# Performance work log

Measured on AMD Instinct MI355X. Metric: run time of the kernel, lower is better.

## Reference

```python
import jax, jax.numpy as jnp
import numpy as np

VOCAB, D = 100000, 300
B, L = 256, 1000
H, C = 512, 5


def setup_inputs() -> dict:
    key = jax.random.key(0)
    ks = jax.random.split(key, 9)
    emb = jax.random.normal(ks[0], (VOCAB, D), dtype=jnp.float32) * 0.1
    W1 = jax.random.normal(ks[1], (D, H), dtype=jnp.float32) * (1.0 / np.sqrt(D))
    b1 = jnp.zeros((H,), dtype=jnp.float32)
    W2 = jax.random.normal(ks[2], (H, H), dtype=jnp.float32) * (1.0 / np.sqrt(H))
    b2 = jnp.zeros((H,), dtype=jnp.float32)
    W3 = jax.random.normal(ks[3], (H, C), dtype=jnp.float32) * (1.0 / np.sqrt(H))
    b3 = jnp.zeros((C,), dtype=jnp.float32)
    docs = jax.random.randint(ks[4], (B, L), 0, VOCAB, dtype=jnp.int32)
    doc_lens = jax.random.randint(ks[5], (B,), 1, L + 1, dtype=jnp.int32)
    return {"embeddings": emb, "W1": W1, "b1": b1, "W2": W2, "b2": b2,
            "W3": W3, "b3": b3, "docs": docs, "doc_lens": doc_lens}


def reference(embeddings, W1, b1, W2, b2, W3, b3, docs, doc_lens):
    # Fused gather + segment-mean: [B, L, D] -> [B, D]
    gathered = embeddings[docs]                       # [B, L, D]
    avg = gathered.sum(axis=1) / doc_lens.astype(jnp.float32)[:, None]  # [B, D]
    # MLP: in -> hidden (ReLU) -> hidden (ReLU) -> classes
    h = jax.nn.relu(avg @ W1 + b1)
    h = jax.nn.relu(h @ W2 + b2)
    return h @ W3 + b3                                # [B, C]
```

## Files before the change

### kernel.cpp

```cpp
#include <hip/hip_runtime.h>

#define VOCAB 100000
#define D     300
#define B     256
#define L     1000
#define H     512
#define C     5

#define D4    (D / 4)
#define NG    8
#define GL    80
#define RPG   (L / NG)
#define NT    (NG * GL)
#define KS1   (D / 4)
#define KS2   (H / 4)

__global__ __launch_bounds__(NT, 3) void dan_fused_kernel(
    const float* __restrict__ emb, const int* __restrict__ docs,
    const int* __restrict__ dlen,
    const float* __restrict__ W1, const float* __restrict__ b1,
    const float* __restrict__ W2, const float* __restrict__ b2,
    const float* __restrict__ W3, const float* __restrict__ b3,
    float* __restrict__ out) {
  const int b = blockIdx.x;
  const int t = threadIdx.x;

  __shared__ int    sidx[L];
  __shared__ float4 sred[NG][D4];
  __shared__ float4 s_in4[D4];
  __shared__ float  s_h1[H];
  __shared__ float  s_h2[H];
  __shared__ float  s_comb[4][H];
  __shared__ float  s_len;

  if (t < L / 4)
    reinterpret_cast<int4*>(sidx)[t] =
        reinterpret_cast<const int4*>(docs + (size_t)b * L)[t];
  if (t == NT - 1) s_len = (float)dlen[b];
  __syncthreads();

  const int g = t / GL;
  const int lane = t - g * GL;
  if (lane < D4) {
    float ax = 0.f, ay = 0.f, az = 0.f, aw = 0.f;
    const int base = g * RPG;
#pragma unroll 2
    for (int i = 0; i < RPG; i += 5) {
      const float4 v0 =
          reinterpret_cast<const float4*>(emb + (size_t)sidx[base + i + 0] * D)[lane];
      const float4 v1 =
          reinterpret_cast<const float4*>(emb + (size_t)sidx[base + i + 1] * D)[lane];
      const float4 v2 =
          reinterpret_cast<const float4*>(emb + (size_t)sidx[base + i + 2] * D)[lane];
      const float4 v3 =
          reinterpret_cast<const float4*>(emb + (size_t)sidx[base + i + 3] * D)[lane];
      const float4 v4 =
          reinterpret_cast<const float4*>(emb + (size_t)sidx[base + i + 4] * D)[lane];
      ax += v0.x; ay += v0.y; az += v0.z; aw += v0.w;
      ax += v1.x; ay += v1.y; az += v1.z; aw += v1.w;
      ax += v2.x; ay += v2.y; az += v2.z; aw += v2.w;
      ax += v3.x; ay += v3.y; az += v3.z; aw += v3.w;
      ax += v4.x; ay += v4.y; az += v4.z; aw += v4.w;
    }
    sred[g][lane] = make_float4(ax, ay, az, aw);
  }
  __syncthreads();

  if (t < D4) {
    float ax = 0.f, ay = 0.f, az = 0.f, aw = 0.f;
#pragma unroll
    for (int gg = 0; gg < NG; ++gg) {
      const float4 v = sred[gg][t];
      ax += v.x; ay += v.y; az += v.z; aw += v.w;
    }
    const float inv = 1.f / s_len;
    s_in4[t] = make_float4(ax * inv, ay * inv, az * inv, aw * inv);
  }
  __syncthreads();

  const float* s_in = reinterpret_cast<const float*>(s_in4);
  const int cg = t & 127;
  const int ks = (t >> 7) & 3;

  if (t < 512) {
    float ax = 0.f, ay = 0.f, az = 0.f, aw = 0.f;
    const int k0 = ks * KS1;
#pragma unroll 1
    for (int i = 0; i < KS1; i += 15) {
      float4 w[15];
#pragma unroll
      for (int j = 0; j < 15; ++j)
        w[j] = *reinterpret_cast<const float4*>(&W1[(k0 + i + j) * H + 4 * cg]);
#pragma unroll
      for (int j = 0; j < 15; ++j) {
        const float x = s_in[k0 + i + j];
        ax += x * w[j].x; ay += x * w[j].y; az += x * w[j].z; aw += x * w[j].w;
      }
    }
    *reinterpret_cast<float4*>(&s_comb[ks][4 * cg]) =
        make_float4(ax, ay, az, aw);
  }
  __syncthreads();
  if (t < H) {
    const float v =
        s_comb[0][t] + s_comb[1][t] + s_comb[2][t] + s_comb[3][t] + b1[t];
    s_h1[t] = fmaxf(v, 0.f);
  }
  __syncthreads();

  if (t < 512) {
    float ax = 0.f, ay = 0.f, az = 0.f, aw = 0.f;
    const int k0 = ks * KS2;
#pragma unroll 1
    for (int i = 0; i < KS2; i += 16) {
      float4 w[16];
#pragma unroll
      for (int j = 0; j < 16; ++j)
        w[j] = *reinterpret_cast<const float4*>(&W2[(k0 + i + j) * H + 4 * cg]);
#pragma unroll
      for (int j = 0; j < 16; ++j) {
        const float x = s_h1[k0 + i + j];
        ax += x * w[j].x; ay += x * w[j].y; az += x * w[j].z; aw += x * w[j].w;
      }
    }
    *reinterpret_cast<float4*>(&s_comb[ks][4 * cg]) =
        make_float4(ax, ay, az, aw);
  }
  __syncthreads();
  if (t < H) {
    const float v =
        s_comb[0][t] + s_comb[1][t] + s_comb[2][t] + s_comb[3][t] + b2[t];
    s_h2[t] = fmaxf(v, 0.f);
  }
  __syncthreads();

  const int wv = t >> 6;
  const int ln = t & 63;
  if (wv < C) {
    float a = 0.f;
#pragma unroll
    for (int i = 0; i < H / 64; ++i) {
      const int h = i * 64 + ln;
      a += s_h2[h] * W3[h * C + wv];
    }
#pragma unroll
    for (int off = 32; off > 0; off >>= 1) a += __shfl_down(a, off);
    if (ln == 0) out[b * C + wv] = a + b3[wv];
  }
}

extern "C" void kernel_launch(void* const* d_in, const int* in_sizes, int n_in,
                              void* d_out, int out_size, void* d_ws,
                              size_t ws_size, hipStream_t stream) {
  const float* emb  = (const float*)d_in[0];
  const float* W1   = (const float*)d_in[1];
  const float* b1   = (const float*)d_in[2];
  const float* W2   = (const float*)d_in[3];
  const float* b2   = (const float*)d_in[4];
  const float* W3   = (const float*)d_in[5];
  const float* b3   = (const float*)d_in[6];
  const int*   docs = (const int*)d_in[7];
  const int*   dlen = (const int*)d_in[8];
  float* out = (float*)d_out;

  dan_fused_kernel<<<B, NT, 0, stream>>>(emb, docs, dlen, W1, b1, W2, b2, W3,
                                         b3, out);
}
```

Baseline: 68.65 us.

## Split fused kernel into gather-mean and batched tiled MLP kernels

Splits the single per-document fused kernel into four kernels: gather+mean, a layer-1 GEMM, a layer-2 GEMM and a small head. The GEMM kernels tile 16 documents by 32 output columns, so each W1/W2 load is reused across 16 documents instead of every block streaming the full weight matrices. The gather loop is also made explicitly double-buffered with sched barriers to keep more loads in flight. The cost is three extra kernel launches and round-trips of the intermediates through global workspace memory.

```diff
diff --git a/kernel.cpp b/kernel.cpp
--- a/kernel.cpp
+++ b/kernel.cpp
@@ -7,61 +7,67 @@
 #define H     512
 #define C     5
 
-#define D4    (D / 4)
+#define D4    75
 #define NG    8
 #define GL    80
-#define RPG   (L / NG)
-#define NT    (NG * GL)
-#define KS1   (D / 4)
-#define KS2   (H / 4)
-
-__global__ __launch_bounds__(NT, 3) void dan_fused_kernel(
-    const float* __restrict__ emb, const int* __restrict__ docs,
-    const int* __restrict__ dlen,
-    const float* __restrict__ W1, const float* __restrict__ b1,
-    const float* __restrict__ W2, const float* __restrict__ b2,
-    const float* __restrict__ W3, const float* __restrict__ b3,
-    float* __restrict__ out) {
+#define RPG   125
+#define NT    640
+
+#define WS_AVG 0
+#define WS_H1  (B * D)
+#define WS_H2  (WS_H1 + B * H)
+
+__global__ __launch_bounds__(NT)
+__attribute__((amdgpu_waves_per_eu(2, 3)))
+void gather_mean_kernel(const float* __restrict__ emb,
+                        const int* __restrict__ docs,
+                        const int* __restrict__ dlen,
+                        float* __restrict__ avg) {
   const int b = blockIdx.x;
   const int t = threadIdx.x;
 
   __shared__ int    sidx[L];
   __shared__ float4 sred[NG][D4];
-  __shared__ float4 s_in4[D4];
-  __shared__ float  s_h1[H];
-  __shared__ float  s_h2[H];
-  __shared__ float  s_comb[4][H];
-  __shared__ float  s_len;
 
   if (t < L / 4)
     reinterpret_cast<int4*>(sidx)[t] =
         reinterpret_cast<const int4*>(docs + (size_t)b * L)[t];
-  if (t == NT - 1) s_len = (float)dlen[b];
   __syncthreads();
 
   const int g = t / GL;
   const int lane = t - g * GL;
+  const float4* ep4 = reinterpret_cast<const float4*>(emb);
+
   if (lane < D4) {
+    const int base = g * RPG;
     float ax = 0.f, ay = 0.f, az = 0.f, aw = 0.f;
-    const int base = g * RPG;
-#pragma unroll 2
-    for (int i = 0; i < RPG; i += 5) {
-      const float4 v0 =
-          reinterpret_cast<const float4*>(emb + (size_t)sidx[base + i + 0] * D)[lane];
-      const float4 v1 =
-          reinterpret_cast<const float4*>(emb + (size_t)sidx[base + i + 1] * D)[lane];
-      const float4 v2 =
-          reinterpret_cast<const float4*>(emb + (size_t)sidx[base + i + 2] * D)[lane];
-      const float4 v3 =
-          reinterpret_cast<const float4*>(emb + (size_t)sidx[base + i + 3] * D)[lane];
-      const float4 v4 =
-          reinterpret_cast<const float4*>(emb + (size_t)sidx[base + i + 4] * D)[lane];
-      ax += v0.x; ay += v0.y; az += v0.z; aw += v0.w;
-      ax += v1.x; ay += v1.y; az += v1.z; aw += v1.w;
-      ax += v2.x; ay += v2.y; az += v2.z; aw += v2.w;
-      ax += v3.x; ay += v3.y; az += v3.z; aw += v3.w;
-      ax += v4.x; ay += v4.y; az += v4.z; aw += v4.w;
-    }
+    float4 va[5], vb[5];
+
+    auto loadb = [&](float4* v, int off) {
+#pragma unroll
+      for (int j = 0; j < 5; ++j) {
+        const int r = sidx[base + off + j] * D4 + lane;
+        v[j] = ep4[r];
+      }
+    };
+    auto accb = [&](const float4* v) {
+#pragma unroll
+      for (int j = 0; j < 5; ++j) {
+        ax += v[j].x; ay += v[j].y; az += v[j].z; aw += v[j].w;
+      }
+    };
+
+    loadb(va, 0);
+#pragma unroll 1
+    for (int p = 0; p < 12; ++p) {
+      loadb(vb, 10 * p + 5);
+      __builtin_amdgcn_sched_barrier(0);
+      accb(va);
+      loadb(va, 10 * p + 10);
+      __builtin_amdgcn_sched_barrier(0);
+      accb(vb);
+    }
+    accb(va);
     sred[g][lane] = make_float4(ax, ay, az, aw);
   }
   __syncthreads();
@@ -73,79 +79,137 @@
       const float4 v = sred[gg][t];
       ax += v.x; ay += v.y; az += v.z; aw += v.w;
     }
-    const float inv = 1.f / s_len;
-    s_in4[t] = make_float4(ax * inv, ay * inv, az * inv, aw * inv);
-  }
-  __syncthreads();
-
-  const float* s_in = reinterpret_cast<const float*>(s_in4);
-  const int cg = t & 127;
-  const int ks = (t >> 7) & 3;
-
-  if (t < 512) {
-    float ax = 0.f, ay = 0.f, az = 0.f, aw = 0.f;
-    const int k0 = ks * KS1;
+    const float inv = 1.f / (float)dlen[b];
+    reinterpret_cast<float4*>(avg + (size_t)b * D)[t] =
+        make_float4(ax * inv, ay * inv, az * inv, aw * inv);
+  }
+}
+
+__global__ __launch_bounds__(512)
+__attribute__((amdgpu_waves_per_eu(2, 4)))
+void l1_kernel(const float* __restrict__ avg, const float* __restrict__ W1,
+               const float* __restrict__ b1, float* __restrict__ h1) {
+  const int dq = blockIdx.x;
+  const int cq = blockIdx.y;
+  const int t = threadIdx.x;
+  const int cg = t & 7;
+  const int doc = (t >> 3) & 15;
+  const int ks = t >> 7;
+
+  __shared__ __align__(16) float s_avg[16][D];
+  __shared__ __align__(16) float s_comb[4][16][32];
+
+  for (int i = t; i < 16 * D4; i += 512) {
+    const int dd = i / D4, c4 = i - dd * D4;
+    reinterpret_cast<float4*>(&s_avg[dd][0])[c4] =
+        reinterpret_cast<const float4*>(avg + (size_t)(dq * 16 + dd) * D)[c4];
+  }
+  __syncthreads();
+
+  const int c0 = cq * 32 + cg * 4;
+  const int k0 = ks * 75;
+  float ax = 0.f, ay = 0.f, az = 0.f, aw = 0.f;
 #pragma unroll 1
-    for (int i = 0; i < KS1; i += 15) {
-      float4 w[15];
-#pragma unroll
-      for (int j = 0; j < 15; ++j)
-        w[j] = *reinterpret_cast<const float4*>(&W1[(k0 + i + j) * H + 4 * cg]);
-#pragma unroll
-      for (int j = 0; j < 15; ++j) {
-        const float x = s_in[k0 + i + j];
-        ax += x * w[j].x; ay += x * w[j].y; az += x * w[j].z; aw += x * w[j].w;
-      }
-    }
-    *reinterpret_cast<float4*>(&s_comb[ks][4 * cg]) =
-        make_float4(ax, ay, az, aw);
-  }
-  __syncthreads();
-  if (t < H) {
-    const float v =
-        s_comb[0][t] + s_comb[1][t] + s_comb[2][t] + s_comb[3][t] + b1[t];
-    s_h1[t] = fmaxf(v, 0.f);
-  }
-  __syncthreads();
-
-  if (t < 512) {
-    float ax = 0.f, ay = 0.f, az = 0.f, aw = 0.f;
-    const int k0 = ks * KS2;
+  for (int i0 = 0; i0 < 75; i0 += 15) {
+    float4 w[15];
+    float x[15];
+#pragma unroll
+    for (int j = 0; j < 15; ++j)
+      w[j] = *reinterpret_cast<const float4*>(&W1[(size_t)(k0 + i0 + j) * H + c0]);
+#pragma unroll
+    for (int j = 0; j < 15; ++j) x[j] = s_avg[doc][k0 + i0 + j];
+    __builtin_amdgcn_sched_barrier(0);
+#pragma unroll
+    for (int j = 0; j < 15; ++j) {
+      ax += x[j] * w[j].x; ay += x[j] * w[j].y;
+      az += x[j] * w[j].z; aw += x[j] * w[j].w;
+    }
+  }
+  *reinterpret_cast<float4*>(&s_comb[ks][doc][cg * 4]) =
+      make_float4(ax, ay, az, aw);
+  __syncthreads();
+
+  {
+    const int dd = t >> 5, col = t & 31;
+    const float v = s_comb[0][dd][col] + s_comb[1][dd][col] +
+                    s_comb[2][dd][col] + s_comb[3][dd][col] +
+                    b1[cq * 32 + col];
+    h1[(size_t)(dq * 16 + dd) * H + cq * 32 + col] = fmaxf(v, 0.f);
+  }
+}
+
+__global__ __launch_bounds__(512)
+__attribute__((amdgpu_waves_per_eu(2, 4)))
+void l2_kernel(const float* __restrict__ h1, const float* __restrict__ W2,
+               const float* __restrict__ b2, float* __restrict__ h2) {
+  const int dq = blockIdx.x;
+  const int cq = blockIdx.y;
+  const int t = threadIdx.x;
+  const int cg = t & 7;
+  const int doc = (t >> 3) & 15;
+  const int ks = t >> 7;
+
+  __shared__ __align__(16) float s_h[16][H + 4];
+  __shared__ __align__(16) float s_comb[4][16][32];
+
+  for (int i = t; i < 16 * (H / 4); i += 512) {
+    const int dd = i >> 7, c4 = i & 127;
+    reinterpret_cast<float4*>(&s_h[dd][0])[c4] =
+        reinterpret_cast<const float4*>(h1 + (size_t)(dq * 16 + dd) * H)[c4];
+  }
+  __syncthreads();
+
+  const int c0 = cq * 32 + cg * 4;
+  const int k0 = ks * 128;
+  float ax = 0.f, ay = 0.f, az = 0.f, aw = 0.f;
 #pragma unroll 1
-    for (int i = 0; i < KS2; i += 16) {
-      float4 w[16];
-#pragma unroll
-      for (int j = 0; j < 16; ++j)
-        w[j] = *reinterpret_cast<const float4*>(&W2[(k0 + i + j) * H + 4 * cg]);
-#pragma unroll
-      for (int j = 0; j < 16; ++j) {
-        const float x = s_h1[k0 + i + j];
-        ax += x * w[j].x; ay += x * w[j].y; az += x * w[j].z; aw += x * w[j].w;
-      }
-    }
-    *reinterpret_cast<float4*>(&s_comb[ks][4 * cg]) =
-        make_float4(ax, ay, az, aw);
-  }
-  __syncthreads();
-  if (t < H) {
-    const float v =
-        s_comb[0][t] + s_comb[1][t] + s_comb[2][t] + s_comb[3][t] + b2[t];
-    s_h2[t] = fmaxf(v, 0.f);
-  }
-  __syncthreads();
-
-  const int wv = t >> 6;
-  const int ln = t & 63;
-  if (wv < C) {
-    float a = 0.f;
-#pragma unroll
-    for (int i = 0; i < H / 64; ++i) {
-      const int h = i * 64 + ln;
-      a += s_h2[h] * W3[h * C + wv];
-    }
+  for (int i0 = 0; i0 < 128; i0 += 16) {
+    float4 w[16];
+    float x[16];
+#pragma unroll
+    for (int j = 0; j < 16; ++j)
+      w[j] = *reinterpret_cast<const float4*>(&W2[(size_t)(k0 + i0 + j) * H + c0]);
+#pragma unroll
+    for (int j = 0; j < 16; ++j) x[j] = s_h[doc][k0 + i0 + j];
+    __builtin_amdgcn_sched_barrier(0);
+#pragma unroll
+    for (int j = 0; j < 16; ++j) {
+      ax += x[j] * w[j].x; ay += x[j] * w[j].y;
+      az += x[j] * w[j].z; aw += x[j] * w[j].w;
+    }
+  }
+  *reinterpret_cast<float4*>(&s_comb[ks][doc][cg * 4]) =
+      make_float4(ax, ay, az, aw);
+  __syncthreads();
+
+  {
+    const int dd = t >> 5, col = t & 31;
+    const float v = s_comb[0][dd][col] + s_comb[1][dd][col] +
+                    s_comb[2][dd][col] + s_comb[3][dd][col] +
+                    b2[cq * 32 + col];
+    h2[(size_t)(dq * 16 + dd) * H + cq * 32 + col] = fmaxf(v, 0.f);
+  }
+}
+
+__global__ __launch_bounds__(64) void head_kernel(
+    const float* __restrict__ h2, const float* __restrict__ W3,
+    const float* __restrict__ b3, float* __restrict__ out) {
+  const int b = blockIdx.x;
+  const int l = threadIdx.x;
+  float acc[C] = {0.f, 0.f, 0.f, 0.f, 0.f};
+#pragma unroll
+  for (int i = 0; i < H / 64; ++i) {
+    const int h = i * 64 + l;
+    const float v = h2[(size_t)b * H + h];
+#pragma unroll
+    for (int c = 0; c < C; ++c) acc[c] += v * W3[h * C + c];
+  }
+#pragma unroll
+  for (int c = 0; c < C; ++c) {
+    float a = acc[c];
 #pragma unroll
     for (int off = 32; off > 0; off >>= 1) a += __shfl_down(a, off);
-    if (ln == 0) out[b * C + wv] = a + b3[wv];
+    if (l == 0) out[b * C + c] = a + b3[c];
   }
 }
 
@@ -163,6 +227,14 @@
   const int*   dlen = (const int*)d_in[8];
   float* out = (float*)d_out;
 
-  dan_fused_kernel<<<B, NT, 0, stream>>>(emb, docs, dlen, W1, b1, W2, b2, W3,
-                                         b3, out);
-}
+  float* ws = (float*)d_ws;
+  float* avg = ws + WS_AVG;
+  float* h1  = ws + WS_H1;
+  float* h2  = ws + WS_H2;
+
+  gather_mean_kernel<<<B, NT, 0, stream>>>(emb, docs, dlen, avg);
+  dim3 gl(16, 16);
+  l1_kernel<<<gl, 512, 0, stream>>>(avg, W1, b1, h1);
+  l2_kernel<<<gl, 512, 0, stream>>>(h1, W2, b2, h2);
+  head_kernel<<<B, 64, 0, stream>>>(h2, W3, b3, out);
+}
```

New measurement: 74.04 us. 7.8% more time.
